# Kernel optimization log

Hardware: AMD Instinct MI355X
Metric: run time of the kernel (lower is better)

## Reference

```python
import jax, jax.numpy as jnp
import numpy as np

N_FEATURES = 2048


def setup_inputs() -> dict:
    key = jax.random.key(0)
    kx, kd, kl, ku = jax.random.split(key, 4)
    x = jax.random.normal(kx, (32, 1024, N_FEATURES), dtype=jnp.float32)
    # torch initializes these params to zeros; use small random values so
    # gradients/flow are non-degenerate while keeping M diagonally dominant.
    d = 0.1 * jax.random.normal(kd, (N_FEATURES,), dtype=jnp.float32)
    l = 0.1 * jax.random.normal(kl, (N_FEATURES - 1,), dtype=jnp.float32)
    u = 0.1 * jax.random.normal(ku, (N_FEATURES - 1,), dtype=jnp.float32)
    return {"x": x, "d": d, "l": l, "u": u}


def reference(x, d, l, u):
    # Build tridiagonal matrix M (faithful to the torch dense construction)
    diag = jax.nn.softplus(d) + 2.0          # [n]
    off_l = jnp.tanh(l)                       # [n-1], subdiagonal
    off_u = jnp.tanh(u)                       # [n-1], superdiagonal
    M = jnp.diag(diag) + jnp.diag(off_l, -1) + jnp.diag(off_u, 1)  # [n, n]
    # Solve M @ y_t = x^T for each batch: x [B, S, n] -> x_t [B, n, S]
    x_t = jnp.swapaxes(x, -2, -1)
    y_t = jnp.linalg.solve(M, x_t)            # M broadcasts over batch
    return jnp.swapaxes(y_t, -2, -1)          # [B, S, n]
```

## Files before the change

kernel.cpp:

```cpp
#include <hip/hip_runtime.h>
#include <math.h>

#define NF 2048
#define ROWS (32 * 1024)
#define CELLS (NF / 4)
#define PHASES 8
#define NBLOCKS 2048
#define BLKTHREADS 512

typedef float f32x4 __attribute__((ext_vector_type(4)));

__device__ __forceinline__ float dpp_up1(float v, float oldv) {
  return __int_as_float(__builtin_amdgcn_update_dpp(
      __float_as_int(oldv), __float_as_int(v), 0x138, 0xF, 0xF, false));
}
__device__ __forceinline__ float dpp_dn1(float v, float oldv) {
  return __int_as_float(__builtin_amdgcn_update_dpp(
      __float_as_int(oldv), __float_as_int(v), 0x130, 0xF, 0xF, false));
}
__device__ __forceinline__ float bcast_lane(float v, int lane) {
  return __int_as_float(__builtin_amdgcn_readlane(__float_as_int(v), lane));
}

__global__ __launch_bounds__(256) void precompute_kernel(
    const float* __restrict__ d, const float* __restrict__ l,
    const float* __restrict__ u, float* __restrict__ wsg,
    float* __restrict__ wsc, float* __restrict__ wsib) {
  __shared__ float diag_s[NF], tl_s[NF], tu_s[NF], b_s[NF];
  const int tid = threadIdx.x;

  for (int i = tid; i < NF; i += 256) {
    float dv = d[i];
    float sp = (dv > 20.f) ? dv : log1pf(expf(dv));
    diag_s[i] = sp + 2.f;
    tl_s[i] = (i < NF - 1) ? tanhf(l[i]) : 0.f;
    tu_s[i] = (i < NF - 1) ? tanhf(u[i]) : 0.f;
  }
  __syncthreads();

  if (tid < 64) {
    const int lane = tid;
    float T00 = 1.f, T01 = 0.f, T10 = 0.f, T11 = 1.f;
#pragma unroll 1
    for (int j = 0; j < 32; ++j) {
      int i = lane * 32 + j;
      float a = diag_s[i];
      float b = (i > 0) ? -tl_s[i - 1] * tu_s[i - 1] : 0.f;
      float n00 = a * T00 + b * T10;
      float n01 = a * T01 + b * T11;
      T10 = T00; T11 = T01; T00 = n00; T01 = n01;
      float s = 1.f / (fabsf(T00) + fabsf(T01) + 1e-30f);
      T00 *= s; T01 *= s; T10 *= s; T11 *= s;
    }
    for (int ofs = 1; ofs < 64; ofs <<= 1) {
      float U00 = __shfl_up(T00, ofs, 64);
      float U01 = __shfl_up(T01, ofs, 64);
      float U10 = __shfl_up(T10, ofs, 64);
      float U11 = __shfl_up(T11, ofs, 64);
      if (lane >= ofs) {
        float n00 = T00 * U00 + T01 * U10;
        float n01 = T00 * U01 + T01 * U11;
        float n10 = T10 * U00 + T11 * U10;
        float n11 = T10 * U01 + T11 * U11;
        T00 = n00; T01 = n01; T10 = n10; T11 = n11;
        float s = 1.f / (fabsf(T00) + fabsf(T01) + 1e-30f);
        T00 *= s; T01 *= s; T10 *= s; T11 *= s;
      }
    }
    float p1 = __shfl_up(T00, 1, 64);
    float p2 = __shfl_up(T10, 1, 64);
    float bp = (lane == 0) ? 1.f : p1 / p2;
#pragma unroll 1
    for (int j = 0; j < 32; ++j) {
      int i = lane * 32 + j;
      float km1 = (i > 0) ? tl_s[i - 1] * tu_s[i - 1] : 0.f;
      float bv = diag_s[i] - km1 / bp;
      b_s[i] = bv;
      bp = bv;
    }
  }
  __syncthreads();

  for (int i = tid; i < NF; i += 256) {
    float invb = 1.f / b_s[i];
    wsg[i] = (i > 0) ? -tl_s[i - 1] / b_s[i - 1] : 0.f;
    wsc[i] = (i < NF - 1) ? -tu_s[i] * invb : 0.f;
    wsib[i] = invb;
  }
}

__global__ __launch_bounds__(BLKTHREADS) void solve_kernel(
    const float* __restrict__ x, const float* __restrict__ wsg,
    const float* __restrict__ wsc, const float* __restrict__ wsib,
    float* __restrict__ y) {
  __shared__ float4 g_s[CELLS], c_s[CELLS], ib_s[CELLS];

  const int lane = threadIdx.x & 63;
  const unsigned wave = (blockIdx.x * BLKTHREADS + threadIdx.x) >> 6;
  const unsigned o0 = (2u * wave) * (NF / 4) + lane;
  const unsigned o1 = o0 + (NF / 4);
  const float4* xb = (const float4*)x;
  float4* yb = (float4*)y;

  float4 v0[PHASES], v1[PHASES];
#pragma unroll
  for (int t = 0; t < PHASES; ++t) {
    v0[t] = xb[o0 + t * 64];
    v1[t] = xb[o1 + t * 64];
  }

  for (int t = threadIdx.x; t < CELLS; t += BLKTHREADS) {
    g_s[t] = ((const float4*)wsg)[t];
    c_s[t] = ((const float4*)wsc)[t];
    ib_s[t] = ((const float4*)wsib)[t];
  }
  __syncthreads();

  const float4* gs = &g_s[lane];
  const float4* cs = &c_s[lane];
  const float4* ibs = &ib_s[lane];

  {
    float ct0 = 0.f, ct1 = 0.f;
#pragma unroll
    for (int t = 0; t < PHASES; ++t) {
      float4 g = gs[t * 64];
      float4 d0 = v0[t], d1 = v1[t];
      d0.y = fmaf(g.y, d0.x, d0.y);
      d0.z = fmaf(g.z, d0.y, d0.z);
      d0.w = fmaf(g.w, d0.z, d0.w);
      d1.y = fmaf(g.y, d1.x, d1.y);
      d1.z = fmaf(g.z, d1.y, d1.z);
      d1.w = fmaf(g.w, d1.z, d1.w);
      float A = g.x * g.y * g.z * g.w;
      float A2 = A * dpp_up1(A, 1.f);
      float B0 = fmaf(A, dpp_up1(d0.w, 0.f), d0.w);
      float B1 = fmaf(A, dpp_up1(d1.w, 0.f), d1.w);
      B0 = fmaf(A2, ct0, B0);
      B1 = fmaf(A2, ct1, B1);
      float vin0 = dpp_up1(B0, ct0);
      float vin1 = dpp_up1(B1, ct1);
      ct0 = bcast_lane(B0, 63);
      ct1 = bcast_lane(B1, 63);
      float p = g.x;
      d0.x = fmaf(p, vin0, d0.x);
      d1.x = fmaf(p, vin1, d1.x);
      p *= g.y;
      d0.y = fmaf(p, vin0, d0.y);
      d1.y = fmaf(p, vin1, d1.y);
      p *= g.z;
      d0.z = fmaf(p, vin0, d0.z);
      d1.z = fmaf(p, vin1, d1.z);
      p *= g.w;
      d0.w = fmaf(p, vin0, d0.w);
      d1.w = fmaf(p, vin1, d1.w);
      v0[t] = d0;
      v1[t] = d1;
    }
  }

  {
    float ct0 = 0.f, ct1 = 0.f;
#pragma unroll
    for (int t = PHASES - 1; t >= 0; --t) {
      float4 c = cs[t * 64];
      float4 ib = ibs[t * 64];
      float4 d0 = v0[t], d1 = v1[t];
      float4 w0, w1;
      w0.w = ib.w * d0.w;
      w0.z = fmaf(c.z, w0.w, ib.z * d0.z);
      w0.y = fmaf(c.y, w0.z, ib.y * d0.y);
      w0.x = fmaf(c.x, w0.y, ib.x * d0.x);
      w1.w = ib.w * d1.w;
      w1.z = fmaf(c.z, w1.w, ib.z * d1.z);
      w1.y = fmaf(c.y, w1.z, ib.y * d1.y);
      w1.x = fmaf(c.x, w1.y, ib.x * d1.x);
      float A = c.x * c.y * c.z * c.w;
      float A2 = A * dpp_dn1(A, 1.f);
      float B0 = fmaf(A, dpp_dn1(w0.x, 0.f), w0.x);
      float B1 = fmaf(A, dpp_dn1(w1.x, 0.f), w1.x);
      B0 = fmaf(A2, ct0, B0);
      B1 = fmaf(A2, ct1, B1);
      float vin0 = dpp_dn1(B0, ct0);
      float vin1 = dpp_dn1(B1, ct1);
      ct0 = bcast_lane(B0, 0);
      ct1 = bcast_lane(B1, 0);
      float p = c.w;
      w0.w = fmaf(p, vin0, w0.w);
      w1.w = fmaf(p, vin1, w1.w);
      p *= c.z;
      w0.z = fmaf(p, vin0, w0.z);
      w1.z = fmaf(p, vin1, w1.z);
      p *= c.y;
      w0.y = fmaf(p, vin0, w0.y);
      w1.y = fmaf(p, vin1, w1.y);
      p *= c.x;
      w0.x = fmaf(p, vin0, w0.x);
      w1.x = fmaf(p, vin1, w1.x);
      __builtin_nontemporal_store(*(const f32x4*)&w0, (f32x4*)&yb[o0 + t * 64]);
      __builtin_nontemporal_store(*(const f32x4*)&w1, (f32x4*)&yb[o1 + t * 64]);
    }
  }
}

extern "C" void kernel_launch(void* const* d_in, const int* in_sizes, int n_in,
                              void* d_out, int out_size, void* d_ws,
                              size_t ws_size, hipStream_t stream) {
  const float* x = (const float*)d_in[0];
  const float* d = (const float*)d_in[1];
  const float* l = (const float*)d_in[2];
  const float* u = (const float*)d_in[3];
  float* out = (float*)d_out;

  float* wsg = (float*)d_ws;
  float* wsc = wsg + NF;
  float* wsib = wsc + NF;

  precompute_kernel<<<1, 256, 0, stream>>>(d, l, u, wsg, wsc, wsib);
  solve_kernel<<<NBLOCKS, BLKTHREADS, 0, stream>>>(x, wsg, wsc, wsib, out);
}
```

Measured before the change: 113.5 us.

## Process one row per wave and read coefficients from global instead of LDS

Each wave now solves one row instead of two, halving per-thread register usage, and the launch uses 8192 blocks of 256 threads with a min-8-blocks-per-CU hint. The LDS staging of the coefficient arrays and the block barrier are removed; coefficients are read directly from global memory, where they should stay cached. This aims to raise occupancy and the number of loads in flight for this memory-bound solve. In exchange, each row carries its own DPP/readlane carry chain, so there is less instruction-level parallelism per wave and more coefficient loads per row.

Result: slower. 119.5 us (+5.3%).

```diff
diff --git a/kernel.cpp b/kernel.cpp
--- a/kernel.cpp
+++ b/kernel.cpp
@@ -3,10 +3,9 @@
 
 #define NF 2048
 #define ROWS (32 * 1024)
-#define CELLS (NF / 4)
 #define PHASES 8
-#define NBLOCKS 2048
-#define BLKTHREADS 512
+#define NBLOCKS 8192
+#define BLKTHREADS 256
 
 typedef float f32x4 __attribute__((ext_vector_type(4)));
 
@@ -89,116 +88,71 @@
   }
 }
 
-__global__ __launch_bounds__(BLKTHREADS) void solve_kernel(
+__global__ __launch_bounds__(BLKTHREADS, 8) void solve_kernel(
     const float* __restrict__ x, const float* __restrict__ wsg,
     const float* __restrict__ wsc, const float* __restrict__ wsib,
     float* __restrict__ y) {
-  __shared__ float4 g_s[CELLS], c_s[CELLS], ib_s[CELLS];
-
   const int lane = threadIdx.x & 63;
-  const unsigned wave = (blockIdx.x * BLKTHREADS + threadIdx.x) >> 6;
-  const unsigned o0 = (2u * wave) * (NF / 4) + lane;
-  const unsigned o1 = o0 + (NF / 4);
+  const unsigned row = (blockIdx.x * BLKTHREADS + threadIdx.x) >> 6;
+  const unsigned o = row * (NF / 4) + lane;
   const float4* xb = (const float4*)x;
   float4* yb = (float4*)y;
+  const float4* gb = (const float4*)wsg;
+  const float4* cb = (const float4*)wsc;
+  const float4* ibb = (const float4*)wsib;
 
-  float4 v0[PHASES], v1[PHASES];
+  float4 v[PHASES];
 #pragma unroll
-  for (int t = 0; t < PHASES; ++t) {
-    v0[t] = xb[o0 + t * 64];
-    v1[t] = xb[o1 + t * 64];
-  }
-
-  for (int t = threadIdx.x; t < CELLS; t += BLKTHREADS) {
-    g_s[t] = ((const float4*)wsg)[t];
-    c_s[t] = ((const float4*)wsc)[t];
-    ib_s[t] = ((const float4*)wsib)[t];
-  }
-  __syncthreads();
-
-  const float4* gs = &g_s[lane];
-  const float4* cs = &c_s[lane];
-  const float4* ibs = &ib_s[lane];
+  for (int t = 0; t < PHASES; ++t) v[t] = xb[o + t * 64];
 
   {
-    float ct0 = 0.f, ct1 = 0.f;
+    float ct = 0.f;
 #pragma unroll
     for (int t = 0; t < PHASES; ++t) {
-      float4 g = gs[t * 64];
-      float4 d0 = v0[t], d1 = v1[t];
-      d0.y = fmaf(g.y, d0.x, d0.y);
-      d0.z = fmaf(g.z, d0.y, d0.z);
-      d0.w = fmaf(g.w, d0.z, d0.w);
-      d1.y = fmaf(g.y, d1.x, d1.y);
-      d1.z = fmaf(g.z, d1.y, d1.z);
-      d1.w = fmaf(g.w, d1.z, d1.w);
+      float4 g = gb[lane + t * 64];
+      float4 dv = v[t];
+      dv.y = fmaf(g.y, dv.x, dv.y);
+      dv.z = fmaf(g.z, dv.y, dv.z);
+      dv.w = fmaf(g.w, dv.z, dv.w);
       float A = g.x * g.y * g.z * g.w;
       float A2 = A * dpp_up1(A, 1.f);
-      float B0 = fmaf(A, dpp_up1(d0.w, 0.f), d0.w);
-      float B1 = fmaf(A, dpp_up1(d1.w, 0.f), d1.w);
-      B0 = fmaf(A2, ct0, B0);
-      B1 = fmaf(A2, ct1, B1);
-      float vin0 = dpp_up1(B0, ct0);
-      float vin1 = dpp_up1(B1, ct1);
-      ct0 = bcast_lane(B0, 63);
-      ct1 = bcast_lane(B1, 63);
+      float B = fmaf(A, dpp_up1(dv.w, 0.f), dv.w);
+      B = fmaf(A2, ct, B);
+      float vin = dpp_up1(B, ct);
+      ct = bcast_lane(B, 63);
       float p = g.x;
-      d0.x = fmaf(p, vin0, d0.x);
-      d1.x = fmaf(p, vin1, d1.x);
-      p *= g.y;
-      d0.y = fmaf(p, vin0, d0.y);
-      d1.y = fmaf(p, vin1, d1.y);
-      p *= g.z;
-      d0.z = fmaf(p, vin0, d0.z);
-      d1.z = fmaf(p, vin1, d1.z);
-      p *= g.w;
-      d0.w = fmaf(p, vin0, d0.w);
-      d1.w = fmaf(p, vin1, d1.w);
-      v0[t] = d0;
-      v1[t] = d1;
+      dv.x = fmaf(p, vin, dv.x);
+      p *= g.y; dv.y = fmaf(p, vin, dv.y);
+      p *= g.z; dv.z = fmaf(p, vin, dv.z);
+      p *= g.w; dv.w = fmaf(p, vin, dv.w);
+      v[t] = dv;
     }
   }
 
   {
-    float ct0 = 0.f, ct1 = 0.f;
+    float ct = 0.f;
 #pragma unroll
     for (int t = PHASES - 1; t >= 0; --t) {
-      float4 c = cs[t * 64];
-      float4 ib = ibs[t * 64];
-      float4 d0 = v0[t], d1 = v1[t];
-      float4 w0, w1;
-      w0.w = ib.w * d0.w;
-      w0.z = fmaf(c.z, w0.w, ib.z * d0.z);
-      w0.y = fmaf(c.y, w0.z, ib.y * d0.y);
-      w0.x = fmaf(c.x, w0.y, ib.x * d0.x);
-      w1.w = ib.w * d1.w;
-      w1.z = fmaf(c.z, w1.w, ib.z * d1.z);
-      w1.y = fmaf(c.y, w1.z, ib.y * d1.y);
-      w1.x = fmaf(c.x, w1.y, ib.x * d1.x);
+      float4 c = cb[lane + t * 64];
+      float4 ib = ibb[lane + t * 64];
+      float4 dv = v[t];
+      float4 w;
+      w.w = ib.w * dv.w;
+      w.z = fmaf(c.z, w.w, ib.z * dv.z);
+      w.y = fmaf(c.y, w.z, ib.y * dv.y);
+      w.x = fmaf(c.x, w.y, ib.x * dv.x);
       float A = c.x * c.y * c.z * c.w;
       float A2 = A * dpp_dn1(A, 1.f);
-      float B0 = fmaf(A, dpp_dn1(w0.x, 0.f), w0.x);
-      float B1 = fmaf(A, dpp_dn1(w1.x, 0.f), w1.x);
-      B0 = fmaf(A2, ct0, B0);
-      B1 = fmaf(A2, ct1, B1);
-      float vin0 = dpp_dn1(B0, ct0);
-      float vin1 = dpp_dn1(B1, ct1);
-      ct0 = bcast_lane(B0, 0);
-      ct1 = bcast_lane(B1, 0);
+      float B = fmaf(A, dpp_dn1(w.x, 0.f), w.x);
+      B = fmaf(A2, ct, B);
+      float vin = dpp_dn1(B, ct);
+      ct = bcast_lane(B, 0);
       float p = c.w;
-      w0.w = fmaf(p, vin0, w0.w);
-      w1.w = fmaf(p, vin1, w1.w);
-      p *= c.z;
-      w0.z = fmaf(p, vin0, w0.z);
-      w1.z = fmaf(p, vin1, w1.z);
-      p *= c.y;
-      w0.y = fmaf(p, vin0, w0.y);
-      w1.y = fmaf(p, vin1, w1.y);
-      p *= c.x;
-      w0.x = fmaf(p, vin0, w0.x);
-      w1.x = fmaf(p, vin1, w1.x);
-      __builtin_nontemporal_store(*(const f32x4*)&w0, (f32x4*)&yb[o0 + t * 64]);
-      __builtin_nontemporal_store(*(const f32x4*)&w1, (f32x4*)&yb[o1 + t * 64]);
+      w.w = fmaf(p, vin, w.w);
+      p *= c.z; w.z = fmaf(p, vin, w.z);
+      p *= c.y; w.y = fmaf(p, vin, w.y);
+      p *= c.x; w.x = fmaf(p, vin, w.x);
+      __builtin_nontemporal_store(*(const f32x4*)&w, (f32x4*)&yb[o + t * 64]);
     }
   }
 }
```
